# Performance work log

Measured on AMD Instinct MI355X. Metric: run time of the kernel, lower is better.

The kernel has to match this reference:

```python
import jax, jax.numpy as jnp
import numpy as np

B, N, NT, DX, DY, H, OUT = 8, 1024, 256, 2, 2, 16, 16


def setup_inputs() -> dict:
    key = jax.random.key(0)
    ks = jax.random.split(key, 6)
    return {
        "x_ctx": jax.random.normal(ks[0], (B, N, DX), dtype=jnp.float32),
        "y_ctx": jax.random.normal(ks[1], (B, N, DY), dtype=jnp.float32),
        "x_trg": jax.random.normal(ks[2], (B, NT, DX), dtype=jnp.float32),
        "W1": jax.random.normal(ks[3], (DX + 2 * DY, H), dtype=jnp.float32) * 0.4,
        "b1": jnp.zeros((H,), dtype=jnp.float32),
        "W2": jax.random.normal(ks[4], (H, OUT), dtype=jnp.float32) * 0.25,
        "b2": jnp.zeros((OUT,), dtype=jnp.float32),
    }


def reference(x_ctx, y_ctx, x_trg, W1, b1, W2, b2):
    # Pairwise differences over the fully-connected context 'graph': [B,N,N,Dx]
    x_diff = x_ctx[:, None, :, :] - x_ctx[:, :, None, :]
    b, n = x_ctx.shape[0], x_ctx.shape[1]
    dy = y_ctx.shape[-1]
    # y tilings (broadcast instead of .repeat; concatenation materializes them)
    y_tile1 = jnp.broadcast_to(y_ctx[:, None, :, :], (b, n, n, dy))
    y_tile2 = jnp.broadcast_to(y_ctx[:, :, None, :], (b, n, n, dy))
    ctx = jnp.concatenate([x_diff, y_tile1, y_tile2], axis=-1)  # [B,N,N,Dx+2Dy]
    # Deepset: pointwise MLP (phi) then mean-pool over context axis
    h = jax.nn.relu(jnp.einsum("bnmf,fh->bnmh", ctx, W1) + b1)
    phi = jnp.einsum("bnmh,ho->bnmo", h, W2) + b2
    r = jnp.mean(phi, axis=2)  # [B,N,OUT]
    return r
```

## Files before the change

### kernel.cpp

```cpp
#include <hip/hip_runtime.h>


constexpr int NN = 1024;

__global__ __launch_bounds__(512, 2) void te_enc(
    const float* __restrict__ x_ctx,
    const float* __restrict__ y_ctx,
    const float* __restrict__ W1,
    const float* __restrict__ b1,
    const float* __restrict__ W2,
    const float* __restrict__ b2,
    float* __restrict__ out)
{
    __shared__ float lds[16384];

    const int t    = threadIdx.x;
    const int wave = t >> 6;
    const int lane = t & 63;
    const int g    = lane & 3;
    const int nsub = lane >> 2;
    const int b    = blockIdx.x >> 5;
    const int n0   = (blockIdx.x & 31) << 5;

    const float4 w10 = *(const float4*)(W1 +  0 + 4*g);
    const float4 w11 = *(const float4*)(W1 + 16 + 4*g);
    const float4 w12 = *(const float4*)(W1 + 32 + 4*g);
    const float4 w13 = *(const float4*)(W1 + 48 + 4*g);
    const float4 w14 = *(const float4*)(W1 + 64 + 4*g);
    const float4 w15 = *(const float4*)(W1 + 80 + 4*g);
    const float4 b1c = *(const float4*)(b1 + 4*g);

    {
        const int mm = t >> 2;
        #pragma unroll
        for (int rep = 0; rep < 8; ++rep) {
            const int m = rep * 128 + mm;
            const float2 xm = *(const float2*)(x_ctx + (b * NN + m) * 2);
            const float2 ym = *(const float2*)(y_ctx + (b * NN + m) * 2);
            float4 u;
            u.x = xm.x*w10.x + xm.y*w11.x + ym.x*w12.x + ym.y*w13.x;
            u.y = xm.x*w10.y + xm.y*w11.y + ym.x*w12.y + ym.y*w13.y;
            u.z = xm.x*w10.z + xm.y*w11.z + ym.x*w12.z + ym.y*w13.z;
            u.w = xm.x*w10.w + xm.y*w11.w + ym.x*w12.w + ym.y*w13.w;
            *(float4*)(lds + m * 16 + 4 * g) = u;
        }
    }

    const int n1 = n0 + nsub;
    const int n2 = n1 + 16;
    float4 v1, v2;
    {
        const float2 xn = *(const float2*)(x_ctx + (b * NN + n1) * 2);
        const float2 yn = *(const float2*)(y_ctx + (b * NN + n1) * 2);
        v1.x = b1c.x - xn.x*w10.x - xn.y*w11.x + yn.x*w14.x + yn.y*w15.x;
        v1.y = b1c.y - xn.x*w10.y - xn.y*w11.y + yn.x*w14.y + yn.y*w15.y;
        v1.z = b1c.z - xn.x*w10.z - xn.y*w11.z + yn.x*w14.z + yn.y*w15.z;
        v1.w = b1c.w - xn.x*w10.w - xn.y*w11.w + yn.x*w14.w + yn.y*w15.w;
    }
    {
        const float2 xn = *(const float2*)(x_ctx + (b * NN + n2) * 2);
        const float2 yn = *(const float2*)(y_ctx + (b * NN + n2) * 2);
        v2.x = b1c.x - xn.x*w10.x - xn.y*w11.x + yn.x*w14.x + yn.y*w15.x;
        v2.y = b1c.y - xn.x*w10.y - xn.y*w11.y + yn.x*w14.y + yn.y*w15.y;
        v2.z = b1c.z - xn.x*w10.z - xn.y*w11.z + yn.x*w14.z + yn.y*w15.z;
        v2.w = b1c.w - xn.x*w10.w - xn.y*w11.w + yn.x*w14.w + yn.y*w15.w;
    }

    __syncthreads();

    float4 s1 = {0.f, 0.f, 0.f, 0.f};
    float4 s2 = {0.f, 0.f, 0.f, 0.f};
    const float* up = lds + wave * 2048 + 4 * g;
    #pragma unroll 4
    for (int i = 0; i < 128; ++i) {
        const float4 u = *(const float4*)(up + i * 16);
        s1.x += fabsf(u.x + v1.x);
        s1.y += fabsf(u.y + v1.y);
        s1.z += fabsf(u.z + v1.z);
        s1.w += fabsf(u.w + v1.w);
        s2.x += fabsf(u.x + v2.x);
        s2.y += fabsf(u.y + v2.y);
        s2.z += fabsf(u.z + v2.z);
        s2.w += fabsf(u.w + v2.w);
    }

    __syncthreads();

    {
        const int base = ((wave * 64 + lane) * 2) * 4;
        *(float4*)(lds + base)     = s1;
        *(float4*)(lds + base + 4) = s2;
    }
    if (wave == 0) {
        *(float4*)(lds + 4096 + n1 % 32 * 0 + (nsub)      * 16 + 4 * g) = v1;
        *(float4*)(lds + 4096 + (nsub + 16) * 16 + 4 * g) = v2;
    }
    if (t < 256) lds[4608 + t] = W2[t];
    if (t < 16)  lds[4864 + t] = b2[t];
    if (t < 64)  lds[4880 + t] = W1[t];

    {
        const float4 xa = *(const float4*)(x_ctx + b * 2048 + t * 4);
        const float4 ya = *(const float4*)(y_ctx + b * 2048 + t * 4);
        float sxx = xa.x + xa.z;
        float sxy = xa.y + xa.w;
        float syx = ya.x + ya.z;
        float syy = ya.y + ya.w;
        #pragma unroll
        for (int off = 32; off > 0; off >>= 1) {
            sxx += __shfl_down(sxx, off);
            sxy += __shfl_down(sxy, off);
            syx += __shfl_down(syx, off);
            syy += __shfl_down(syy, off);
        }
        if (lane == 0) {
            float4 bs = {sxx, sxy, syx, syy};
            *(float4*)(lds + 4944 + wave * 4) = bs;
        }
    }
    __syncthreads();

    if (t < 128) {
        const int l = t >> 1;
        const int p = t & 1;
        float4 acc = {0.f, 0.f, 0.f, 0.f};
        #pragma unroll
        for (int w = 0; w < 8; ++w) {
            const float4 q = *(const float4*)(lds + ((w * 64 + l) * 2 + p) * 4);
            acc.x += q.x; acc.y += q.y; acc.z += q.z; acc.w += q.w;
        }
        float4 bs = {0.f, 0.f, 0.f, 0.f};
        #pragma unroll
        for (int w = 0; w < 8; ++w) {
            const float4 q = *(const float4*)(lds + 4944 + w * 4);
            bs.x += q.x; bs.y += q.y; bs.z += q.z; bs.w += q.w;
        }
        const int nsf = (l >> 2) + 16 * p;
        const int gf  = l & 3;
        const int c   = 4 * gf;
        float4 su;
        su.x = bs.x*lds[4880+c  ] + bs.y*lds[4896+c  ] + bs.z*lds[4912+c  ] + bs.w*lds[4928+c  ];
        su.y = bs.x*lds[4880+c+1] + bs.y*lds[4896+c+1] + bs.z*lds[4912+c+1] + bs.w*lds[4928+c+1];
        su.z = bs.x*lds[4880+c+2] + bs.y*lds[4896+c+2] + bs.z*lds[4912+c+2] + bs.w*lds[4928+c+2];
        su.w = bs.x*lds[4880+c+3] + bs.y*lds[4896+c+3] + bs.z*lds[4912+c+3] + bs.w*lds[4928+c+3];
        const float4 vv = *(const float4*)(lds + 4096 + nsf * 16 + c);
        const float k = 0.5f / 1024.0f;
        float4 r;
        r.x = (acc.x + su.x) * k + 0.5f * vv.x;
        r.y = (acc.y + su.y) * k + 0.5f * vv.y;
        r.z = (acc.z + su.z) * k + 0.5f * vv.z;
        r.w = (acc.w + su.w) * k + 0.5f * vv.w;
        *(float4*)(lds + 4976 + nsf * 16 + c) = r;
    }
    __syncthreads();

    {
        const int j = t >> 4;
        const int o = t & 15;
        const float* sf = lds + 4976 + j * 16;
        const float* w2 = lds + 4608;
        float acc = lds[4864 + o];
        #pragma unroll
        for (int h = 0; h < 16; ++h)
            acc += sf[h] * w2[h * 16 + o];
        out[(b * NN + n0 + j) * 16 + o] = acc;
    }
}

extern "C" void kernel_launch(void* const* d_in, const int* in_sizes, int n_in,
                              void* d_out, int out_size, void* d_ws, size_t ws_size,
                              hipStream_t stream) {
    const float* x_ctx = (const float*)d_in[0];
    const float* y_ctx = (const float*)d_in[1];
    const float* W1 = (const float*)d_in[3];
    const float* b1 = (const float*)d_in[4];
    const float* W2 = (const float*)d_in[5];
    const float* b2 = (const float*)d_in[6];
    float* out = (float*)d_out;

    te_enc<<<256, 512, 0, stream>>>(x_ctx, y_ctx, W1, b1, W2, b2, out);
}
```

Before: 75.75 us.

## Retile pairwise loop so each thread reuses loaded u across eight targets

Restructures the inner abs-sum loop. Each thread now holds 8 target v vectors in registers and walks 32 context rows, so every LDS float4 load of u feeds 8 targets instead of 2. The per-target v values are precomputed into LDS by all threads. The partial sums go to a padded LDS spill area and are reduced across 32 slices. In exchange it uses more registers (8 accumulators plus 8 v vectors), more LDS, an extra barrier, and a longer cross-slice reduction.

New measurement: 77.33 us. 1.02x slower.

```diff
diff --git a/kernel.cpp b/kernel.cpp
--- a/kernel.cpp
+++ b/kernel.cpp
@@ -2,6 +2,15 @@
 
 
 constexpr int NN = 1024;
+
+#define SPILL_STRIDE 528
+#define V_OFF   16896
+#define W2_OFF  17408
+#define B2_OFF  17664
+#define W1_OFF  17680
+#define BS_OFF  17744
+#define SF_OFF  17776
+#define LDS_FLOATS 18288
 
 __global__ __launch_bounds__(512, 2) void te_enc(
     const float* __restrict__ x_ctx,
@@ -12,26 +21,34 @@
     const float* __restrict__ b2,
     float* __restrict__ out)
 {
-    __shared__ float lds[16384];
+    __shared__ float lds[LDS_FLOATS];
 
     const int t    = threadIdx.x;
     const int wave = t >> 6;
     const int lane = t & 63;
-    const int g    = lane & 3;
-    const int nsub = lane >> 2;
     const int b    = blockIdx.x >> 5;
     const int n0   = (blockIdx.x & 31) << 5;
 
-    const float4 w10 = *(const float4*)(W1 +  0 + 4*g);
-    const float4 w11 = *(const float4*)(W1 + 16 + 4*g);
-    const float4 w12 = *(const float4*)(W1 + 32 + 4*g);
-    const float4 w13 = *(const float4*)(W1 + 48 + 4*g);
-    const float4 w14 = *(const float4*)(W1 + 64 + 4*g);
-    const float4 w15 = *(const float4*)(W1 + 80 + 4*g);
-    const float4 b1c = *(const float4*)(b1 + 4*g);
+    if (t < 256) lds[W2_OFF + t] = W2[t];
+    if (t < 16)  lds[B2_OFF + t] = b2[t];
+    if (t < 64)  lds[W1_OFF + t] = W1[t];
 
     {
-        const int mm = t >> 2;
+        const int nt = t >> 4, h = t & 15;
+        const int n  = n0 + nt;
+        const float2 xn = *(const float2*)(x_ctx + (b * NN + n) * 2);
+        const float2 yn = *(const float2*)(y_ctx + (b * NN + n) * 2);
+        lds[V_OFF + nt * 16 + h] =
+            b1[h] - xn.x * W1[h] - xn.y * W1[16 + h]
+                  + yn.x * W1[64 + h] + yn.y * W1[80 + h];
+    }
+
+    {
+        const int g = t & 3, mm = t >> 2;
+        const float4 w10 = *(const float4*)(W1 +  0 + 4 * g);
+        const float4 w11 = *(const float4*)(W1 + 16 + 4 * g);
+        const float4 w12 = *(const float4*)(W1 + 32 + 4 * g);
+        const float4 w13 = *(const float4*)(W1 + 48 + 4 * g);
         #pragma unroll
         for (int rep = 0; rep < 8; ++rep) {
             const int m = rep * 128 + mm;
@@ -45,59 +62,6 @@
             *(float4*)(lds + m * 16 + 4 * g) = u;
         }
     }
-
-    const int n1 = n0 + nsub;
-    const int n2 = n1 + 16;
-    float4 v1, v2;
-    {
-        const float2 xn = *(const float2*)(x_ctx + (b * NN + n1) * 2);
-        const float2 yn = *(const float2*)(y_ctx + (b * NN + n1) * 2);
-        v1.x = b1c.x - xn.x*w10.x - xn.y*w11.x + yn.x*w14.x + yn.y*w15.x;
-        v1.y = b1c.y - xn.x*w10.y - xn.y*w11.y + yn.x*w14.y + yn.y*w15.y;
-        v1.z = b1c.z - xn.x*w10.z - xn.y*w11.z + yn.x*w14.z + yn.y*w15.z;
-        v1.w = b1c.w - xn.x*w10.w - xn.y*w11.w + yn.x*w14.w + yn.y*w15.w;
-    }
-    {
-        const float2 xn = *(const float2*)(x_ctx + (b * NN + n2) * 2);
-        const float2 yn = *(const float2*)(y_ctx + (b * NN + n2) * 2);
-        v2.x = b1c.x - xn.x*w10.x - xn.y*w11.x + yn.x*w14.x + yn.y*w15.x;
-        v2.y = b1c.y - xn.x*w10.y - xn.y*w11.y + yn.x*w14.y + yn.y*w15.y;
-        v2.z = b1c.z - xn.x*w10.z - xn.y*w11.z + yn.x*w14.z + yn.y*w15.z;
-        v2.w = b1c.w - xn.x*w10.w - xn.y*w11.w + yn.x*w14.w + yn.y*w15.w;
-    }
-
-    __syncthreads();
-
-    float4 s1 = {0.f, 0.f, 0.f, 0.f};
-    float4 s2 = {0.f, 0.f, 0.f, 0.f};
-    const float* up = lds + wave * 2048 + 4 * g;
-    #pragma unroll 4
-    for (int i = 0; i < 128; ++i) {
-        const float4 u = *(const float4*)(up + i * 16);
-        s1.x += fabsf(u.x + v1.x);
-        s1.y += fabsf(u.y + v1.y);
-        s1.z += fabsf(u.z + v1.z);
-        s1.w += fabsf(u.w + v1.w);
-        s2.x += fabsf(u.x + v2.x);
-        s2.y += fabsf(u.y + v2.y);
-        s2.z += fabsf(u.z + v2.z);
-        s2.w += fabsf(u.w + v2.w);
-    }
-
-    __syncthreads();
-
-    {
-        const int base = ((wave * 64 + lane) * 2) * 4;
-        *(float4*)(lds + base)     = s1;
-        *(float4*)(lds + base + 4) = s2;
-    }
-    if (wave == 0) {
-        *(float4*)(lds + 4096 + n1 % 32 * 0 + (nsub)      * 16 + 4 * g) = v1;
-        *(float4*)(lds + 4096 + (nsub + 16) * 16 + 4 * g) = v2;
-    }
-    if (t < 256) lds[4608 + t] = W2[t];
-    if (t < 16)  lds[4864 + t] = b2[t];
-    if (t < 64)  lds[4880 + t] = W1[t];
 
     {
         const float4 xa = *(const float4*)(x_ctx + b * 2048 + t * 4);
@@ -114,52 +78,85 @@
             syy += __shfl_down(syy, off);
         }
         if (lane == 0) {
-            float4 bs = {sxx, sxy, syx, syy};
-            *(float4*)(lds + 4944 + wave * 4) = bs;
+            float4 bsv = {sxx, sxy, syx, syy};
+            *(float4*)(lds + BS_OFF + wave * 4) = bsv;
         }
     }
     __syncthreads();
 
+    const int c  = lane & 3;
+    const int ms = lane >> 2;
+    const int ng = wave & 3;
+    const int mh = wave >> 2;
+    float4 v[8];
+    #pragma unroll
+    for (int j = 0; j < 8; ++j)
+        v[j] = *(const float4*)(lds + V_OFF + (ng * 8 + j) * 16 + 4 * c);
+
+    float4 s[8];
+    #pragma unroll
+    for (int j = 0; j < 8; ++j) s[j] = make_float4(0.f, 0.f, 0.f, 0.f);
+
+    const float* up = lds + (mh * 512 + ms) * 16 + 4 * c;
+    #pragma unroll 4
+    for (int i = 0; i < 32; ++i) {
+        const float4 u = *(const float4*)(up + i * 256);
+        #pragma unroll
+        for (int j = 0; j < 8; ++j) {
+            s[j].x += fabsf(u.x + v[j].x);
+            s[j].y += fabsf(u.y + v[j].y);
+            s[j].z += fabsf(u.z + v[j].z);
+            s[j].w += fabsf(u.w + v[j].w);
+        }
+    }
+    __syncthreads();
+
+    {
+        const int slice = mh * 16 + ms;
+        float* sp = lds + slice * SPILL_STRIDE + 4 * c;
+        #pragma unroll
+        for (int j = 0; j < 8; ++j)
+            *(float4*)(sp + (ng * 8 + j) * 16) = s[j];
+    }
+    __syncthreads();
+
     if (t < 128) {
-        const int l = t >> 1;
-        const int p = t & 1;
+        const int nt = t >> 2, h4 = t & 3, hh = h4 * 4;
         float4 acc = {0.f, 0.f, 0.f, 0.f};
         #pragma unroll
-        for (int w = 0; w < 8; ++w) {
-            const float4 q = *(const float4*)(lds + ((w * 64 + l) * 2 + p) * 4);
+        for (int sl = 0; sl < 32; ++sl) {
+            const float4 q = *(const float4*)(lds + sl * SPILL_STRIDE + nt * 16 + hh);
             acc.x += q.x; acc.y += q.y; acc.z += q.z; acc.w += q.w;
         }
-        float4 bs = {0.f, 0.f, 0.f, 0.f};
+        float4 bsum = {0.f, 0.f, 0.f, 0.f};
         #pragma unroll
         for (int w = 0; w < 8; ++w) {
-            const float4 q = *(const float4*)(lds + 4944 + w * 4);
-            bs.x += q.x; bs.y += q.y; bs.z += q.z; bs.w += q.w;
+            const float4 q = *(const float4*)(lds + BS_OFF + w * 4);
+            bsum.x += q.x; bsum.y += q.y; bsum.z += q.z; bsum.w += q.w;
         }
-        const int nsf = (l >> 2) + 16 * p;
-        const int gf  = l & 3;
-        const int c   = 4 * gf;
+        const float* w1r = lds + W1_OFF;
         float4 su;
-        su.x = bs.x*lds[4880+c  ] + bs.y*lds[4896+c  ] + bs.z*lds[4912+c  ] + bs.w*lds[4928+c  ];
-        su.y = bs.x*lds[4880+c+1] + bs.y*lds[4896+c+1] + bs.z*lds[4912+c+1] + bs.w*lds[4928+c+1];
-        su.z = bs.x*lds[4880+c+2] + bs.y*lds[4896+c+2] + bs.z*lds[4912+c+2] + bs.w*lds[4928+c+2];
-        su.w = bs.x*lds[4880+c+3] + bs.y*lds[4896+c+3] + bs.z*lds[4912+c+3] + bs.w*lds[4928+c+3];
-        const float4 vv = *(const float4*)(lds + 4096 + nsf * 16 + c);
+        su.x = bsum.x*w1r[hh  ] + bsum.y*w1r[16+hh  ] + bsum.z*w1r[32+hh  ] + bsum.w*w1r[48+hh  ];
+        su.y = bsum.x*w1r[hh+1] + bsum.y*w1r[16+hh+1] + bsum.z*w1r[32+hh+1] + bsum.w*w1r[48+hh+1];
+        su.z = bsum.x*w1r[hh+2] + bsum.y*w1r[16+hh+2] + bsum.z*w1r[32+hh+2] + bsum.w*w1r[48+hh+2];
+        su.w = bsum.x*w1r[hh+3] + bsum.y*w1r[16+hh+3] + bsum.z*w1r[32+hh+3] + bsum.w*w1r[48+hh+3];
+        const float4 vv = *(const float4*)(lds + V_OFF + nt * 16 + hh);
         const float k = 0.5f / 1024.0f;
         float4 r;
         r.x = (acc.x + su.x) * k + 0.5f * vv.x;
         r.y = (acc.y + su.y) * k + 0.5f * vv.y;
         r.z = (acc.z + su.z) * k + 0.5f * vv.z;
         r.w = (acc.w + su.w) * k + 0.5f * vv.w;
-        *(float4*)(lds + 4976 + nsf * 16 + c) = r;
+        *(float4*)(lds + SF_OFF + nt * 16 + hh) = r;
     }
     __syncthreads();
 
     {
         const int j = t >> 4;
         const int o = t & 15;
-        const float* sf = lds + 4976 + j * 16;
-        const float* w2 = lds + 4608;
-        float acc = lds[4864 + o];
+        const float* sf = lds + SF_OFF + j * 16;
+        const float* w2 = lds + W2_OFF;
+        float acc = lds[B2_OFF + o];
         #pragma unroll
         for (int h = 0; h < 16; ++h)
             acc += sf[h] * w2[h * 16 + o];
```
